# Performance work log

Hardware: AMD Instinct MI355X
Metric: run time of the kernel (lower is better)

Reference implementation:

```python
import jax, jax.numpy as jnp
import numpy as np

B, T, E = 4, 2048, 2048
H, HKV, HD = 16, 8, 128
THETA = 10000.0
SCALE_BASE = 512.0


def _rotate_half(x):
    x1, x2 = jnp.split(x, 2, axis=-1)
    return jnp.concatenate([-x2, x1], axis=-1)


def _xpos_tables(seqlen):
    # cos/sin/scale tables for XPos rotary, all [seqlen, HD], fp32 compute dtype
    half_idx = jnp.arange(0, HD, 2, dtype=jnp.float32)
    inv_freq = 1.0 / (THETA ** (half_idx / HD))            # [HD/2]
    t = jnp.arange(seqlen, dtype=jnp.float32)
    freqs = jnp.outer(t, inv_freq)                          # [seqlen, HD/2]
    emb = jnp.concatenate([freqs, freqs], axis=-1)          # [seqlen, HD]
    cos, sin = jnp.cos(emb), jnp.sin(emb)
    # xpos decay: ((2i + 0.4d)/(1.4d)) ** ((t - L/2)/scale_base)
    scale_vec = (half_idx + 0.4 * HD) / (1.4 * HD)          # [HD/2]
    power = (t - seqlen // 2) / SCALE_BASE                  # [seqlen]
    scale = scale_vec[None, :] ** power[:, None]            # [seqlen, HD/2]
    scale = jnp.concatenate([scale, scale], axis=-1)        # [seqlen, HD]
    return cos, sin, scale


def setup_inputs() -> dict:
    key = jax.random.key(0)
    ks = jax.random.split(key, 5)
    std = 0.02
    return {
        "x": jax.random.normal(ks[0], (B, T, E), dtype=jnp.float32),
        "W_q": jax.random.normal(ks[1], (E, H * HD), dtype=jnp.float32) * std,
        "W_k": jax.random.normal(ks[2], (E, HKV * HD), dtype=jnp.float32) * std,
        "W_v": jax.random.normal(ks[3], (E, HKV * HD), dtype=jnp.float32) * std,
        "W_o": jax.random.normal(ks[4], (E, E), dtype=jnp.float32) * std,
    }


def reference(x, W_q, W_k, W_v, W_o):
    b, t, _ = x.shape
    q = (x @ W_q).reshape(b, t, H, HD)       # [B,T,H,HD]
    k = (x @ W_k).reshape(b, t, HKV, HD)     # [B,T,HKV,HD]
    v = (x @ W_v).reshape(b, t, HKV, HD)
    rep = H // HKV                            # GQA: repeat_interleave over head dim
    k = jnp.repeat(k, rep, axis=2)
    v = jnp.repeat(v, rep, axis=2)

    cos, sin, scale = _xpos_tables(t)         # past_len = 0 (no kv cache)
    cos = cos[None, :, None, :]
    sin = sin[None, :, None, :]
    scale = scale[None, :, None, :]
    q = q * scale
    q = q * cos + _rotate_half(q) * sin
    k = k / scale
    k = k * cos + _rotate_half(k) * sin

    inv_sqrt_d = 1.0 / jnp.sqrt(jnp.float32(HD))
    scores = jnp.einsum('bqhd,bkhd->bhqk', q, k) * inv_sqrt_d  # [B,H,T,T]
    causal = jnp.triu(jnp.ones((t, t), dtype=bool), k=1)
    scores = jnp.where(causal[None, None], -jnp.inf, scores)
    probs = jax.nn.softmax(scores, axis=-1)
    attn = jnp.einsum('bhqk,bkhd->bqhd', probs, v)             # [B,T,H,HD]
    out = attn.reshape(b, t, E) @ W_o
    return out
```

## Files before the change

kernel.cpp:

```cpp
#include <hip/hip_runtime.h>

typedef _Float16 f16;
typedef __attribute__((ext_vector_type(8))) _Float16 f16x8;
typedef __attribute__((ext_vector_type(4))) _Float16 f16x4;
typedef __attribute__((ext_vector_type(4))) float f32x4;
typedef __attribute__((ext_vector_type(16))) float f32x16;
typedef __attribute__((ext_vector_type(4))) unsigned u32x4;

#define T_SEQ 2048
#define NBATCH 4

__device__ __forceinline__ void gld_lds16(const f16* g, f16* l) {
    __builtin_amdgcn_global_load_lds((const __attribute__((address_space(1))) void*)g,
                                     (__attribute__((address_space(3))) void*)l, 16, 0, 0);
}

__device__ __forceinline__ unsigned pk2(float a, float b) {
    __attribute__((ext_vector_type(2))) __fp16 h = __builtin_amdgcn_cvt_pkrtz(a, b);
    return __builtin_bit_cast(unsigned, h);
}

__global__ __launch_bounds__(256) void k_prep(const float* __restrict__ x,
                                              const float* __restrict__ Wq,
                                              const float* __restrict__ Wk,
                                              const float* __restrict__ Wv,
                                              const float* __restrict__ Wo,
                                              f16* __restrict__ xh,
                                              f16* __restrict__ wqkvT,
                                              f16* __restrict__ woT,
                                              float* __restrict__ tab) {
    __shared__ float tile[32][33];
    int bidx = blockIdx.x;
    if (bidx < 16384) {
        int i = bidx * 256 + threadIdx.x;
        float4 v = ((const float4*)x)[i];
        f16x4 o = { (f16)v.x, (f16)v.y, (f16)v.z, (f16)v.w };
        ((f16x4*)xh)[i] = o;
        return;
    }
    bidx -= 16384;
    if (bidx >= 12288) {
        int i = (bidx - 12288) * 256 + threadIdx.x;
        int t = i >> 6, f = i & 63;
        float inv_freq = powf(10000.0f, -(2.0f * f) / 128.0f);
        float ang = (float)t * inv_freq;
        float sv = (2.0f * f + 51.2f) / 179.2f;
        float pw = ((float)t - 1024.0f) / 512.0f;
        tab[i] = cosf(ang);
        tab[131072 + i] = sinf(ang);
        tab[262144 + i] = powf(sv, pw);
        return;
    }
    const float* src; f16* dst; int N, bx, by;
    if (bidx < 4096)      { src = Wq; dst = wqkvT;                      N = 2048; bx = bidx & 63; by = bidx >> 6; }
    else if (bidx < 6144) { src = Wk; dst = wqkvT + (size_t)2048 * 2048; N = 1024; int t2 = bidx - 4096; bx = t2 & 31; by = t2 >> 5; }
    else if (bidx < 8192) { src = Wv; dst = wqkvT + (size_t)3072 * 2048; N = 1024; int t2 = bidx - 6144; bx = t2 & 31; by = t2 >> 5; }
    else                  { src = Wo; dst = woT;                        N = 2048; int t2 = bidx - 8192; bx = t2 & 63; by = t2 >> 6; }
    int n0 = bx * 32, k0 = by * 32;
    int tx = threadIdx.x & 31, ty = threadIdx.x >> 5;
#pragma unroll
    for (int j = 0; j < 32; j += 8)
        tile[ty + j][tx] = src[(size_t)(k0 + ty + j) * N + n0 + tx];
    __syncthreads();
#pragma unroll
    for (int j = 0; j < 32; j += 8)
        dst[(size_t)(n0 + ty + j) * 2048 + k0 + tx] = (f16)tile[tx][ty + j];
}

__global__ __launch_bounds__(256) void k_post(f16* __restrict__ qkv,
                                              f16* __restrict__ vtg,
                                              const float* __restrict__ tab) {
    int bidx = blockIdx.x;
    const int tid = threadIdx.x;
    if (bidx < 1024) {
        const int kt = bidx & 31, bk = bidx >> 5;
        const int b = bk >> 3, kvh = bk & 7;
        __shared__ f16 tile[64][132];
#pragma unroll
        for (int p = 0; p < 4; ++p) {
            int idx = p * 256 + tid;
            int r = idx >> 4, dc = (idx & 15) * 8;
            f16x8 v = *(const f16x8*)(qkv + (size_t)(b * T_SEQ + kt * 64 + r) * 4096 + 3072 + kvh * 128 + dc);
#pragma unroll
            for (int j = 0; j < 8; ++j) tile[r][dc + j] = v[j];
        }
        __syncthreads();
        f16* outb = vtg + (size_t)(bk * 32 + kt) * 8192;
#pragma unroll
        for (int p = 0; p < 4; ++p) {
            int c = p * 256 + tid;
            int kchunk = c >> 7, d = c & 127;
            f16x8 o;
#pragma unroll
            for (int j = 0; j < 8; ++j) o[j] = tile[kchunk * 8 + j][d];
            *(f16x8*)(outb + (size_t)c * 8) = o;
        }
        return;
    }
    int idx = (bidx - 1024) * 256 + tid;
    const int QTOT = NBATCH * T_SEQ * 16 * 64;
    int f, col0, bt;
    bool isQ = idx < QTOT;
    if (isQ) {
        f = idx & 63; int hh = (idx >> 6) & 15; bt = idx >> 10;
        col0 = hh * 128 + f;
    } else {
        int j = idx - QTOT;
        f = j & 63; int hh = (j >> 6) & 7; bt = j >> 9;
        col0 = 2048 + hh * 128 + f;
    }
    int t = bt & (T_SEQ - 1);
    float cs = tab[t * 64 + f], sn = tab[131072 + t * 64 + f], sc = tab[262144 + t * 64 + f];
    float mult = isQ ? sc * 0.08838834764831845f : 1.0f / sc;
    size_t p = (size_t)bt * 4096 + col0;
    float x1 = (float)qkv[p], x2 = (float)qkv[p + 64];
    qkv[p]      = (f16)((x1 * cs - x2 * sn) * mult);
    qkv[p + 64] = (f16)((x2 * cs + x1 * sn) * mult);
}

template <typename OutT>
__global__ __launch_bounds__(512, 1) void k_gemm256(const f16* __restrict__ A,
                                                    const f16* __restrict__ B,
                                                    OutT* __restrict__ C, int M, int N, int K) {
    extern __shared__ char smem[];
    f16* As = (f16*)smem;
    f16* Bs = (f16*)smem + 32768;
    const int tid = threadIdx.x, lane = tid & 63, w = tid >> 6;
    const int wr4 = w >> 1, wc2 = w & 1;
    const int cq = lane & 15, gq = lane >> 4;
    const int nbx = gridDim.x;
    const int bid0 = blockIdx.y * nbx + blockIdx.x;
    const int x = bid0 & 7, idx = bid0 >> 3;
    const int snb = (nbx == 16) ? 3 : 2;
    const int mt = (x >> 1) * 8 + (idx >> snb);
    const int nt = (x & 1) * (nbx >> 1) + (idx & ((nbx >> 1) - 1));
    const int m0 = mt * 256, n0 = nt * 256;
    const int KT = K >> 6;

    f32x4 acc[2][2][2][4] = {};
    f16x8 aL[2][2], aH[2][2], bL[4][2], bH[4][2];

    auto stageA = [&](int buf, int half, int t) {
#pragma unroll
        for (int r = 0; r < 2; ++r) {
            int cb = r * 512 + w * 64;
            int c = cb + lane;
            int row = c >> 3, cc = c & 7;
            gld_lds16(A + (size_t)(m0 + half * 128 + row) * K + t * 64 + ((cc ^ (row & 7)) * 8),
                      As + buf * 16384 + half * 8192 + cb * 8);
        }
    };
    auto stageB = [&](int buf, int half, int t) {
#pragma unroll
        for (int r = 0; r < 2; ++r) {
            int cb = r * 512 + w * 64;
            int c = cb + lane;
            int row = c >> 3, cc = c & 7;
            gld_lds16(B + (size_t)(n0 + half * 128 + row) * K + t * 64 + ((cc ^ (row & 7)) * 8),
                      Bs + buf * 16384 + half * 8192 + cb * 8);
        }
    };
    auto rdA = [&](int buf, int qr, f16x8 a[2][2]) {
#pragma unroll
        for (int mi = 0; mi < 2; ++mi)
#pragma unroll
            for (int ks = 0; ks < 2; ++ks) {
                int R = qr * 128 + wr4 * 32 + mi * 16 + cq;
                a[mi][ks] = *(const f16x8*)&As[buf * 16384 + R * 64 + (((ks * 4 + gq) ^ (cq & 7)) * 8)];
            }
    };
    auto rdB = [&](int buf, int qc, f16x8 b[4][2]) {
#pragma unroll
        for (int ni = 0; ni < 4; ++ni)
#pragma unroll
            for (int ks = 0; ks < 2; ++ks) {
                int R = qc * 128 + wc2 * 64 + ni * 16 + cq;
                b[ni][ks] = *(const f16x8*)&Bs[buf * 16384 + R * 64 + (((ks * 4 + gq) ^ (cq & 7)) * 8)];
            }
    };

    stageA(0, 0, 0); stageB(0, 0, 0); stageB(0, 1, 0); stageA(0, 1, 0);
    if (KT > 1) { stageA(1, 0, 1); stageB(1, 0, 1); stageB(1, 1, 1); }
    asm volatile("s_waitcnt vmcnt(6)");
    __builtin_amdgcn_s_barrier();

#pragma unroll 1
    for (int t = 0; t < KT; ++t) {
        const int buf = t & 1;
        rdA(buf, 0, aL); rdB(buf, 0, bL);
        __builtin_amdgcn_s_setprio(1);
#pragma unroll
        for (int mi = 0; mi < 2; ++mi)
#pragma unroll
            for (int ni = 0; ni < 4; ++ni)
#pragma unroll
                for (int ks = 0; ks < 2; ++ks)
                    acc[0][0][mi][ni] = __builtin_amdgcn_mfma_f32_16x16x32_f16(aL[mi][ks], bL[ni][ks], acc[0][0][mi][ni], 0, 0, 0);
        __builtin_amdgcn_s_setprio(0);
        if (t + 1 < KT) stageA(buf ^ 1, 1, t + 1);
        rdA(buf, 1, aH);
        rdB(buf, 1, bH);
        __builtin_amdgcn_s_setprio(1);
#pragma unroll
        for (int mi = 0; mi < 2; ++mi)
#pragma unroll
            for (int ni = 0; ni < 4; ++ni)
#pragma unroll
                for (int ks = 0; ks < 2; ++ks)
                    acc[1][0][mi][ni] = __builtin_amdgcn_mfma_f32_16x16x32_f16(aH[mi][ks], bL[ni][ks], acc[1][0][mi][ni], 0, 0, 0);
        __builtin_amdgcn_s_setprio(0);
        asm volatile("s_waitcnt lgkmcnt(0)");
        __builtin_amdgcn_s_barrier();
        if (t + 2 < KT) { stageA(buf, 0, t + 2); stageB(buf, 0, t + 2); stageB(buf, 1, t + 2); }
        __builtin_amdgcn_s_setprio(1);
#pragma unroll
        for (int mi = 0; mi < 2; ++mi)
#pragma unroll
            for (int ni = 0; ni < 4; ++ni)
#pragma unroll
                for (int ks = 0; ks < 2; ++ks)
                    acc[1][1][mi][ni] = __builtin_amdgcn_mfma_f32_16x16x32_f16(aH[mi][ks], bH[ni][ks], acc[1][1][mi][ni], 0, 0, 0);
#pragma unroll
        for (int mi = 0; mi < 2; ++mi)
#pragma unroll
            for (int ni = 0; ni < 4; ++ni)
#pragma unroll
                for (int ks = 0; ks < 2; ++ks)
                    acc[0][1][mi][ni] = __builtin_amdgcn_mfma_f32_16x16x32_f16(aL[mi][ks], bH[ni][ks], acc[0][1][mi][ni], 0, 0, 0);
        __builtin_amdgcn_s_setprio(0);
        if (t + 2 < KT)      asm volatile("s_waitcnt vmcnt(6)");
        else                 asm volatile("s_waitcnt vmcnt(0)");
        __builtin_amdgcn_s_barrier();
    }

#pragma unroll
    for (int qr = 0; qr < 2; ++qr)
#pragma unroll
        for (int qc = 0; qc < 2; ++qc)
#pragma unroll
            for (int mi = 0; mi < 2; ++mi)
#pragma unroll
                for (int ni = 0; ni < 4; ++ni)
#pragma unroll
                    for (int i = 0; i < 4; ++i) {
                        int row = m0 + qr * 128 + wr4 * 32 + mi * 16 + gq * 4 + i;
                        int col = n0 + qc * 128 + wc2 * 64 + ni * 16 + cq;
                        C[(size_t)row * N + col] = (OutT)acc[qr][qc][mi][ni][i];
                    }
}

__global__ __launch_bounds__(512) void k_attn(const f16* __restrict__ qkv,
                                              const f16* __restrict__ vtg,
                                              f16* __restrict__ ao) {
    extern __shared__ f16 asmem[];
    const int bid0 = blockIdx.x;
    const int bid = (bid0 & 7) * 32 + (bid0 >> 3);
    const int pr = bid & 7, kvh = (bid >> 3) & 7, b = bid >> 6;
    const int bk = b * 8 + kvh;
    const int tid = threadIdx.x, lane = tid & 63, w = tid >> 6;
    const int w4 = w & 3, hg = w >> 2;
    const int h = kvh * 2 + hg;
    const int l31 = lane & 31, hi = lane >> 5;

    const f16* kbase = qkv + (size_t)b * T_SEQ * 4096 + 2048 + kvh * 128;
    const f16* vbase = vtg + (size_t)bk * 32 * 8192;

    auto stage = [&](int buf, int kt) {
        f16* kb_ = asmem + buf * 16384;
        f16* vb_ = kb_ + 8192;
#pragma unroll
        for (int qq = 0; qq < 2; ++qq) {
            int c = w * 128 + qq * 64 + lane;
            int row = c >> 4;
            int ch = (c & 15) ^ (row & 15);
            gld_lds16(kbase + (size_t)(kt * 64 + row) * 4096 + ch * 8, kb_ + (w * 128 + qq * 64) * 8);
        }
#pragma unroll
        for (int qq = 0; qq < 2; ++qq) {
            int c = w * 128 + qq * 64 + lane;
            gld_lds16(vbase + ((size_t)kt * 1024 + c) * 8, vb_ + (w * 128 + qq * 64) * 8);
        }
    };

#pragma unroll 1
    for (int hf = 0; hf < 2; ++hf) {
        const int qt = hf ? pr : (15 - pr);
        const int q0 = qt * 128;
        const int nkt = 2 * qt + 2;
        const int qrow = q0 + w4 * 32 + l31;

        f16x8 qf[8];
#pragma unroll
        for (int ds = 0; ds < 8; ++ds)
            qf[ds] = *(const f16x8*)(qkv + (size_t)(b * T_SEQ + qrow) * 4096 + h * 128 + ds * 16 + hi * 8);

        f32x16 Ot[4] = {};
        float mrow = -1e30f, lrow = 0.0f;

        stage(0, 0);
        if (nkt > 1) stage(1, 1);

#pragma unroll 1
        for (int kt = 0; kt < nkt; ++kt) {
            const int kb = kt % 3;
            const f16* Kl = asmem + kb * 16384;
            const f16* Vl = Kl + 8192;
            if (kt + 1 < nkt) asm volatile("s_waitcnt vmcnt(4)");
            else              asm volatile("s_waitcnt vmcnt(0)");
            __builtin_amdgcn_s_barrier();

            if (!(kt == 2 * qt + 1 && w4 < 2)) {
                f32x16 St0 = {}, St1 = {};
                __builtin_amdgcn_s_setprio(1);
#pragma unroll
                for (int ds = 0; ds < 8; ++ds) {
                    int slot = (((2 * ds + hi) ^ (l31 & 15)) << 3);
                    f16x8 k0 = *(const f16x8*)&Kl[l31 * 128 + slot];
                    f16x8 k1 = *(const f16x8*)&Kl[(32 + l31) * 128 + slot];
                    St0 = __builtin_amdgcn_mfma_f32_32x32x16_f16(k0, qf[ds], St0, 0, 0, 0);
                    St1 = __builtin_amdgcn_mfma_f32_32x32x16_f16(k1, qf[ds], St1, 0, 0, 0);
                }
                __builtin_amdgcn_s_setprio(0);

                if (kt >= 2 * qt) {
                    int kbase2 = kt * 64;
#pragma unroll
                    for (int r = 0; r < 16; ++r) {
                        int krel = (r & 3) + 8 * (r >> 2) + 4 * hi;
                        if (kbase2 + krel > qrow) St0[r] = -1e30f;
                        if (kbase2 + 32 + krel > qrow) St1[r] = -1e30f;
                    }
                }

                float tm[16];
#pragma unroll
                for (int r = 0; r < 16; ++r) tm[r] = fmaxf(St0[r], St1[r]);
#pragma unroll
                for (int d = 8; d >= 1; d >>= 1)
#pragma unroll
                    for (int r = 0; r < 8; ++r)
                        if (r < d) tm[r] = fmaxf(tm[r], tm[r + d]);
                float tmax = tm[0];
                float mtile = fmaxf(tmax, __shfl_xor(tmax, 32, 64));

                if (!__all((mtile - mrow) <= 8.0f)) {
                    float mnew = fmaxf(mrow, mtile);
                    float fs = __expf(mrow - mnew);
                    mrow = mnew;
                    lrow *= fs;
#pragma unroll
                    for (int dblk = 0; dblk < 4; ++dblk)
#pragma unroll
                        for (int e = 0; e < 16; ++e) Ot[dblk][e] *= fs;
                }
#pragma unroll
                for (int r = 0; r < 16; ++r) {
                    St0[r] = __expf(St0[r] - mrow);
                    St1[r] = __expf(St1[r] - mrow);
                }
                float ts[16];
#pragma unroll
                for (int r = 0; r < 16; ++r) ts[r] = St0[r] + St1[r];
#pragma unroll
                for (int d = 8; d >= 1; d >>= 1)
#pragma unroll
                    for (int r = 0; r < 8; ++r)
                        if (r < d) ts[r] += ts[r + d];
                float tsum = ts[0];
                lrow += tsum + __shfl_xor(tsum, 32, 64);

#define PV_P(o, pos) ((o) < 4 ? St0[((o) & 3) * 4 + (pos)] : St1[((o) & 3) * 4 + (pos)])
#pragma unroll
                for (int s = 0; s < 4; ++s) {
                    unsigned x1 = pk2(PV_P(2 * s, 0), PV_P(2 * s, 1));
                    unsigned x2 = pk2(PV_P(2 * s, 2), PV_P(2 * s, 3));
                    unsigned y1 = pk2(PV_P(2 * s + 1, 0), PV_P(2 * s + 1, 1));
                    unsigned y2 = pk2(PV_P(2 * s + 1, 2), PV_P(2 * s + 1, 3));
                    unsigned sx1 = __shfl_xor(x1, 32, 64);
                    unsigned sx2 = __shfl_xor(x2, 32, 64);
                    unsigned sy1 = __shfl_xor(y1, 32, 64);
                    unsigned sy2 = __shfl_xor(y2, 32, 64);
                    u32x4 pw;
                    pw[0] = hi ? sy1 : x1;
                    pw[1] = hi ? sy2 : x2;
                    pw[2] = hi ? y1 : sx1;
                    pw[3] = hi ? y2 : sx2;
                    f16x8 pa = __builtin_bit_cast(f16x8, pw);
                    __builtin_amdgcn_s_setprio(1);
#pragma unroll
                    for (int dblk = 0; dblk < 4; ++dblk) {
                        f16x8 vb = *(const f16x8*)&Vl[(((2 * s + hi) << 7) + 32 * dblk + l31) << 3];
                        Ot[dblk] = __builtin_amdgcn_mfma_f32_32x32x16_f16(vb, pa, Ot[dblk], 0, 0, 0);
                    }
                    __builtin_amdgcn_s_setprio(0);
                }
#undef PV_P
            }
            __builtin_amdgcn_s_barrier();
            if (kt + 2 < nkt) stage((kt + 2) % 3, kt + 2);
        }

        {
            float inv = 1.0f / lrow;
            size_t rowb = (size_t)(b * T_SEQ + qrow) * 2048 + h * 128;
#pragma unroll
            for (int dblk = 0; dblk < 4; ++dblk)
#pragma unroll
                for (int rg = 0; rg < 4; ++rg) {
                    f16x4 o4 = { (f16)(Ot[dblk][rg * 4 + 0] * inv), (f16)(Ot[dblk][rg * 4 + 1] * inv),
                                 (f16)(Ot[dblk][rg * 4 + 2] * inv), (f16)(Ot[dblk][rg * 4 + 3] * inv) };
                    *(f16x4*)(ao + rowb + dblk * 32 + rg * 8 + hi * 4) = o4;
                }
        }
    }
}

extern "C" void kernel_launch(void* const* d_in, const int* in_sizes, int n_in,
                              void* d_out, int out_size, void* d_ws, size_t ws_size,
                              hipStream_t stream) {
    const float* x  = (const float*)d_in[0];
    const float* Wq = (const float*)d_in[1];
    const float* Wk = (const float*)d_in[2];
    const float* Wv = (const float*)d_in[3];
    const float* Wo = (const float*)d_in[4];
    float* out = (float*)d_out;

    f16* xh    = (f16*)d_ws;
    f16* wqkvT = xh + (size_t)16777216;
    f16* woT   = wqkvT + (size_t)8388608;
    f16* qkv   = woT + (size_t)4194304;
    float* tab = (float*)(qkv + (size_t)33554432);
    f16* ao  = xh;
    f16* vtg = wqkvT;

    hipFuncSetAttribute(reinterpret_cast<const void*>(&k_gemm256<f16>),
                        hipFuncAttributeMaxDynamicSharedMemorySize, 131072);
    hipFuncSetAttribute(reinterpret_cast<const void*>(&k_gemm256<float>),
                        hipFuncAttributeMaxDynamicSharedMemorySize, 131072);
    hipFuncSetAttribute(reinterpret_cast<const void*>(&k_attn),
                        hipFuncAttributeMaxDynamicSharedMemorySize, 98304);

    k_prep<<<29184, 256, 0, stream>>>(x, Wq, Wk, Wv, Wo, xh, wqkvT, woT, tab);
    k_gemm256<f16><<<dim3(16, 32), 512, 131072, stream>>>(xh, wqkvT, qkv, 8192, 4096, 2048);
    k_post<<<50176, 256, 0, stream>>>(qkv, vtg, tab);
    k_attn<<<256, 512, 98304, stream>>>(qkv, vtg, ao);
    k_gemm256<float><<<dim3(8, 32), 512, 131072, stream>>>(ao, woT, out, 8192, 2048, 2048);
}
```

Before: 368.7 us.

## Fuse XPos rotary and V transpose into QKV GEMM epilogue

Removes the separate k_post kernel by adding a specialized QKV GEMM that stages its output tile in LDS. The epilogue then applies XPos rotary with scaling to the Q/K columns and writes the V tiles directly in the transposed layout the attention kernel expects. This drops a full read-modify-write pass over the QKV buffer and one launch. The cost is a longer GEMM epilogue and an extra LDS round trip. The Q/K buffer row stride changes to 3072 and V gets its own workspace region.

Measured after the change: 414.0 us. 12.3% more time.

```diff
diff --git a/kernel.cpp b/kernel.cpp
--- a/kernel.cpp
+++ b/kernel.cpp
@@ -67,55 +67,181 @@
         dst[(size_t)(n0 + ty + j) * 2048 + k0 + tx] = (f16)tile[tx][ty + j];
 }
 
-__global__ __launch_bounds__(256) void k_post(f16* __restrict__ qkv,
-                                              f16* __restrict__ vtg,
-                                              const float* __restrict__ tab) {
-    int bidx = blockIdx.x;
-    const int tid = threadIdx.x;
-    if (bidx < 1024) {
-        const int kt = bidx & 31, bk = bidx >> 5;
-        const int b = bk >> 3, kvh = bk & 7;
-        __shared__ f16 tile[64][132];
-#pragma unroll
-        for (int p = 0; p < 4; ++p) {
-            int idx = p * 256 + tid;
-            int r = idx >> 4, dc = (idx & 15) * 8;
-            f16x8 v = *(const f16x8*)(qkv + (size_t)(b * T_SEQ + kt * 64 + r) * 4096 + 3072 + kvh * 128 + dc);
-#pragma unroll
-            for (int j = 0; j < 8; ++j) tile[r][dc + j] = v[j];
-        }
-        __syncthreads();
-        f16* outb = vtg + (size_t)(bk * 32 + kt) * 8192;
-#pragma unroll
-        for (int p = 0; p < 4; ++p) {
-            int c = p * 256 + tid;
-            int kchunk = c >> 7, d = c & 127;
+__global__ __launch_bounds__(512, 1) void k_gemm_qkv(const f16* __restrict__ A,
+                                                     const f16* __restrict__ B,
+                                                     f16* __restrict__ qkvqk,
+                                                     f16* __restrict__ vtg,
+                                                     const float* __restrict__ tab) {
+    const int M = 8192, N = 4096, K = 2048, nbx = 16;
+    extern __shared__ char smem[];
+    f16* As = (f16*)smem;
+    f16* Bs = (f16*)smem + 32768;
+    const int tid = threadIdx.x, lane = tid & 63, w = tid >> 6;
+    const int wr4 = w >> 1, wc2 = w & 1;
+    const int cq = lane & 15, gq = lane >> 4;
+    const int bid0 = blockIdx.y * nbx + blockIdx.x;
+    const int x = bid0 & 7, idx = bid0 >> 3;
+    const int mt = (x >> 1) * 8 + (idx >> 3);
+    const int nt = (x & 1) * 8 + (idx & 7);
+    const int m0 = mt * 256, n0 = nt * 256;
+    const int KT = K >> 6;
+
+    f32x4 acc[2][2][2][4] = {};
+    f16x8 aL[2][2], aH[2][2], bL[4][2], bH[4][2];
+
+    auto stageA = [&](int buf, int half, int t) {
+#pragma unroll
+        for (int r = 0; r < 2; ++r) {
+            int cb = r * 512 + w * 64;
+            int c = cb + lane;
+            int row = c >> 3, cc = c & 7;
+            gld_lds16(A + (size_t)(m0 + half * 128 + row) * K + t * 64 + ((cc ^ (row & 7)) * 8),
+                      As + buf * 16384 + half * 8192 + cb * 8);
+        }
+    };
+    auto stageB = [&](int buf, int half, int t) {
+#pragma unroll
+        for (int r = 0; r < 2; ++r) {
+            int cb = r * 512 + w * 64;
+            int c = cb + lane;
+            int row = c >> 3, cc = c & 7;
+            gld_lds16(B + (size_t)(n0 + half * 128 + row) * K + t * 64 + ((cc ^ (row & 7)) * 8),
+                      Bs + buf * 16384 + half * 8192 + cb * 8);
+        }
+    };
+    auto rdA = [&](int buf, int qr, f16x8 a[2][2]) {
+#pragma unroll
+        for (int mi = 0; mi < 2; ++mi)
+#pragma unroll
+            for (int ks = 0; ks < 2; ++ks) {
+                int R = qr * 128 + wr4 * 32 + mi * 16 + cq;
+                a[mi][ks] = *(const f16x8*)&As[buf * 16384 + R * 64 + (((ks * 4 + gq) ^ (cq & 7)) * 8)];
+            }
+    };
+    auto rdB = [&](int buf, int qc, f16x8 b[4][2]) {
+#pragma unroll
+        for (int ni = 0; ni < 4; ++ni)
+#pragma unroll
+            for (int ks = 0; ks < 2; ++ks) {
+                int R = qc * 128 + wc2 * 64 + ni * 16 + cq;
+                b[ni][ks] = *(const f16x8*)&Bs[buf * 16384 + R * 64 + (((ks * 4 + gq) ^ (cq & 7)) * 8)];
+            }
+    };
+
+    stageA(0, 0, 0); stageB(0, 0, 0); stageB(0, 1, 0); stageA(0, 1, 0);
+    if (KT > 1) { stageA(1, 0, 1); stageB(1, 0, 1); stageB(1, 1, 1); }
+    asm volatile("s_waitcnt vmcnt(6)");
+    __builtin_amdgcn_s_barrier();
+
+#pragma unroll 1
+    for (int t = 0; t < KT; ++t) {
+        const int buf = t & 1;
+        rdA(buf, 0, aL); rdB(buf, 0, bL);
+        __builtin_amdgcn_s_setprio(1);
+#pragma unroll
+        for (int mi = 0; mi < 2; ++mi)
+#pragma unroll
+            for (int ni = 0; ni < 4; ++ni)
+#pragma unroll
+                for (int ks = 0; ks < 2; ++ks)
+                    acc[0][0][mi][ni] = __builtin_amdgcn_mfma_f32_16x16x32_f16(aL[mi][ks], bL[ni][ks], acc[0][0][mi][ni], 0, 0, 0);
+        __builtin_amdgcn_s_setprio(0);
+        if (t + 1 < KT) stageA(buf ^ 1, 1, t + 1);
+        rdA(buf, 1, aH);
+        rdB(buf, 1, bH);
+        __builtin_amdgcn_s_setprio(1);
+#pragma unroll
+        for (int mi = 0; mi < 2; ++mi)
+#pragma unroll
+            for (int ni = 0; ni < 4; ++ni)
+#pragma unroll
+                for (int ks = 0; ks < 2; ++ks)
+                    acc[1][0][mi][ni] = __builtin_amdgcn_mfma_f32_16x16x32_f16(aH[mi][ks], bL[ni][ks], acc[1][0][mi][ni], 0, 0, 0);
+        __builtin_amdgcn_s_setprio(0);
+        asm volatile("s_waitcnt lgkmcnt(0)");
+        __builtin_amdgcn_s_barrier();
+        if (t + 2 < KT) { stageA(buf, 0, t + 2); stageB(buf, 0, t + 2); stageB(buf, 1, t + 2); }
+        __builtin_amdgcn_s_setprio(1);
+#pragma unroll
+        for (int mi = 0; mi < 2; ++mi)
+#pragma unroll
+            for (int ni = 0; ni < 4; ++ni)
+#pragma unroll
+                for (int ks = 0; ks < 2; ++ks)
+                    acc[1][1][mi][ni] = __builtin_amdgcn_mfma_f32_16x16x32_f16(aH[mi][ks], bH[ni][ks], acc[1][1][mi][ni], 0, 0, 0);
+#pragma unroll
+        for (int mi = 0; mi < 2; ++mi)
+#pragma unroll
+            for (int ni = 0; ni < 4; ++ni)
+#pragma unroll
+                for (int ks = 0; ks < 2; ++ks)
+                    acc[0][1][mi][ni] = __builtin_amdgcn_mfma_f32_16x16x32_f16(aL[mi][ks], bH[ni][ks], acc[0][1][mi][ni], 0, 0, 0);
+        __builtin_amdgcn_s_setprio(0);
+        if (t + 2 < KT)      asm volatile("s_waitcnt vmcnt(6)");
+        else                 asm volatile("s_waitcnt vmcnt(0)");
+        __builtin_amdgcn_s_barrier();
+    }
+
+    f16* Tl = (f16*)smem;
+#pragma unroll
+    for (int qr = 0; qr < 2; ++qr)
+#pragma unroll
+        for (int qc = 0; qc < 2; ++qc)
+#pragma unroll
+            for (int mi = 0; mi < 2; ++mi)
+#pragma unroll
+                for (int ni = 0; ni < 4; ++ni)
+#pragma unroll
+                    for (int i = 0; i < 4; ++i) {
+                        int rl = qr * 128 + wr4 * 32 + mi * 16 + gq * 4 + i;
+                        int cl = qc * 128 + wc2 * 64 + ni * 16 + cq;
+                        Tl[rl * 256 + cl] = (f16)acc[qr][qc][mi][ni][i];
+                    }
+    __syncthreads();
+
+    if (n0 < 3072) {
+        const bool isQ = (n0 < 2048);
+#pragma unroll 1
+        for (int i = 0; i < 16; ++i) {
+            int u = i * 512 + tid;
+            int rl = u >> 5, cc8 = (u & 31) * 8;
+            int brow = m0 + rl;
+            int t = brow & 2047;
+            int col = n0 + cc8;
+            int f0 = col & 63;
+            f16x8 a = *(const f16x8*)&Tl[rl * 256 + cc8];
+            f16x8 bb = *(const f16x8*)&Tl[rl * 256 + (cc8 ^ 64)];
+            const float* cb2 = tab + t * 64 + f0;
+            const bool h2 = (col & 64) != 0;
             f16x8 o;
 #pragma unroll
-            for (int j = 0; j < 8; ++j) o[j] = tile[kchunk * 8 + j][d];
-            *(f16x8*)(outb + (size_t)c * 8) = o;
-        }
-        return;
+            for (int j = 0; j < 8; ++j) {
+                float cs = cb2[j], sn = cb2[131072 + j], g = cb2[262144 + j];
+                float mult = isQ ? g * 0.08838834764831845f : 1.0f / g;
+                float av = (float)a[j], bv = (float)bb[j];
+                float r_ = h2 ? (av * cs + bv * sn) : (av * cs - bv * sn);
+                o[j] = (f16)(r_ * mult);
+            }
+            *(f16x8*)(qkvqk + (size_t)brow * 3072 + col) = o;
+        }
+    } else {
+        const int b_ = m0 >> 11;
+        const int kt0 = (m0 & 2047) >> 6;
+        const int kvh0 = (n0 - 3072) >> 7;
+#pragma unroll 1
+        for (int i = 0; i < 16; ++i) {
+            int o = i * 512 + tid;
+            int kt_l = o >> 11, r = o & 2047;
+            int kvh_l = r >> 10, r2 = r & 1023;
+            int kchunk = r2 >> 7, d = r2 & 127;
+            f16x8 vv;
+#pragma unroll
+            for (int j = 0; j < 8; ++j)
+                vv[j] = Tl[(kt_l * 64 + kchunk * 8 + j) * 256 + kvh_l * 128 + d];
+            int bk = b_ * 8 + kvh0 + kvh_l;
+            *(f16x8*)(vtg + ((size_t)(bk * 32 + kt0 + kt_l)) * 8192 + (size_t)(kchunk * 128 + d) * 8) = vv;
+        }
     }
-    int idx = (bidx - 1024) * 256 + tid;
-    const int QTOT = NBATCH * T_SEQ * 16 * 64;
-    int f, col0, bt;
-    bool isQ = idx < QTOT;
-    if (isQ) {
-        f = idx & 63; int hh = (idx >> 6) & 15; bt = idx >> 10;
-        col0 = hh * 128 + f;
-    } else {
-        int j = idx - QTOT;
-        f = j & 63; int hh = (j >> 6) & 7; bt = j >> 9;
-        col0 = 2048 + hh * 128 + f;
-    }
-    int t = bt & (T_SEQ - 1);
-    float cs = tab[t * 64 + f], sn = tab[131072 + t * 64 + f], sc = tab[262144 + t * 64 + f];
-    float mult = isQ ? sc * 0.08838834764831845f : 1.0f / sc;
-    size_t p = (size_t)bt * 4096 + col0;
-    float x1 = (float)qkv[p], x2 = (float)qkv[p + 64];
-    qkv[p]      = (f16)((x1 * cs - x2 * sn) * mult);
-    qkv[p + 64] = (f16)((x2 * cs + x1 * sn) * mult);
 }
 
 template <typename OutT>
@@ -249,7 +375,7 @@
                     }
 }
 
-__global__ __launch_bounds__(512) void k_attn(const f16* __restrict__ qkv,
+__global__ __launch_bounds__(512) void k_attn(const f16* __restrict__ qkvqk,
                                               const f16* __restrict__ vtg,
                                               f16* __restrict__ ao) {
     extern __shared__ f16 asmem[];
@@ -262,7 +388,7 @@
     const int h = kvh * 2 + hg;
     const int l31 = lane & 31, hi = lane >> 5;
 
-    const f16* kbase = qkv + (size_t)b * T_SEQ * 4096 + 2048 + kvh * 128;
+    const f16* kbase = qkvqk + (size_t)b * T_SEQ * 3072 + 2048 + kvh * 128;
     const f16* vbase = vtg + (size_t)bk * 32 * 8192;
 
     auto stage = [&](int buf, int kt) {
@@ -273,7 +399,7 @@
             int c = w * 128 + qq * 64 + lane;
             int row = c >> 4;
             int ch = (c & 15) ^ (row & 15);
-            gld_lds16(kbase + (size_t)(kt * 64 + row) * 4096 + ch * 8, kb_ + (w * 128 + qq * 64) * 8);
+            gld_lds16(kbase + (size_t)(kt * 64 + row) * 3072 + ch * 8, kb_ + (w * 128 + qq * 64) * 8);
         }
 #pragma unroll
         for (int qq = 0; qq < 2; ++qq) {
@@ -292,7 +418,7 @@
         f16x8 qf[8];
 #pragma unroll
         for (int ds = 0; ds < 8; ++ds)
-            qf[ds] = *(const f16x8*)(qkv + (size_t)(b * T_SEQ + qrow) * 4096 + h * 128 + ds * 16 + hi * 8);
+            qf[ds] = *(const f16x8*)(qkvqk + (size_t)(b * T_SEQ + qrow) * 3072 + h * 128 + ds * 16 + hi * 8);
 
         f32x16 Ot[4] = {};
         float mrow = -1e30f, lrow = 0.0f;
@@ -425,15 +551,15 @@
     const float* Wo = (const float*)d_in[4];
     float* out = (float*)d_out;
 
-    f16* xh    = (f16*)d_ws;
-    f16* wqkvT = xh + (size_t)16777216;
-    f16* woT   = wqkvT + (size_t)8388608;
-    f16* qkv   = woT + (size_t)4194304;
-    float* tab = (float*)(qkv + (size_t)33554432);
-    f16* ao  = xh;
-    f16* vtg = wqkvT;
-
-    hipFuncSetAttribute(reinterpret_cast<const void*>(&k_gemm256<f16>),
+    f16* xh     = (f16*)d_ws;
+    f16* wqkvT  = xh + (size_t)16777216;
+    f16* woT    = wqkvT + (size_t)8388608;
+    f16* qkvqk  = woT + (size_t)4194304;
+    f16* vtg    = qkvqk + (size_t)25165824;
+    float* tab  = (float*)(vtg + (size_t)8388608);
+    f16* ao = xh;
+
+    hipFuncSetAttribute(reinterpret_cast<const void*>(&k_gemm_qkv),
                         hipFuncAttributeMaxDynamicSharedMemorySize, 131072);
     hipFuncSetAttribute(reinterpret_cast<const void*>(&k_gemm256<float>),
                         hipFuncAttributeMaxDynamicSharedMemorySize, 131072);
@@ -441,8 +567,7 @@
                         hipFuncAttributeMaxDynamicSharedMemorySize, 98304);
 
     k_prep<<<29184, 256, 0, stream>>>(x, Wq, Wk, Wv, Wo, xh, wqkvT, woT, tab);
-    k_gemm256<f16><<<dim3(16, 32), 512, 131072, stream>>>(xh, wqkvT, qkv, 8192, 4096, 2048);
-    k_post<<<50176, 256, 0, stream>>>(qkv, vtg, tab);
-    k_attn<<<256, 512, 98304, stream>>>(qkv, vtg, ao);
+    k_gemm_qkv<<<dim3(16, 32), 512, 131072, stream>>>(xh, wqkvT, qkvqk, vtg, tab);
+    k_attn<<<256, 512, 98304, stream>>>(qkvqk, vtg, ao);
     k_gemm256<float><<<dim3(8, 32), 512, 131072, stream>>>(ao, woT, out, 8192, 2048, 2048);
 }
```
